# Kernel optimization log

Hardware: AMD Instinct MI355X
Metric: run time of the kernel (lower is better)

Reference implementation:

```python
import jax, jax.numpy as jnp
import numpy as np
from jax import lax

V, E, F, TL, NS, B = 10000, 150, 200, 7, 4, 2048
PAD_IDX = 1
EPS = 1e-5
SLOPE = 0.01  # nn.LeakyReLU default


def leaky(x):
    return jnp.where(x >= 0, x, SLOPE * x)


def conv1d(x, w, b):
    # x [B,Cin,L], w [Cout,Cin,K] -> [B,Cout,L-K+1]
    y = lax.conv_general_dilated(x, w, (1,), 'VALID',
                                 dimension_numbers=('NCH', 'OIH', 'NCH'))
    return y + b[None, :, None]


def batchnorm(x, g, b):
    # training-mode BatchNorm1d over [B,C,L]: stats over (B,L), biased var
    m = jnp.mean(x, axis=(0, 2), keepdims=True)
    v = jnp.mean((x - m) ** 2, axis=(0, 2), keepdims=True)
    return (x - m) * lax.rsqrt(v + EPS) * g[None, :, None] + b[None, :, None]


def setup_inputs() -> dict:
    key = jax.random.key(0)
    ks = jax.random.split(key, 24)
    s = 0.05
    inp = {
        'text': jax.random.randint(ks[0], (NS * TL, B), 0, V, dtype=jnp.int32).astype(jnp.int64) if False else jax.random.randint(ks[0], (NS * TL, B), 0, V),
        'ith_sentence': 4,
        'idx': 1,
        'emb': jax.random.normal(ks[1], (V, E), jnp.float32) * s,
        'gamma': jnp.ones((F,), jnp.float32),
        'beta': jnp.zeros((F,), jnp.float32),
        'conv1_w': jax.random.normal(ks[2], (F, E, 2), jnp.float32) * s,
        'conv1_b': jax.random.normal(ks[3], (F,), jnp.float32) * s,
        'conv2_w': jax.random.normal(ks[4], (F, F, 2), jnp.float32) * s,
        'conv2_b': jax.random.normal(ks[5], (F,), jnp.float32) * s,
        'conv3_w': jax.random.normal(ks[6], (F, F, 3), jnp.float32) * s,
        'conv3_b': jax.random.normal(ks[7], (F,), jnp.float32) * s,
        'conv4_w': jax.random.normal(ks[8], (F, F, 3), jnp.float32) * s,
        'conv4_b': jax.random.normal(ks[9], (F,), jnp.float32) * s,
        'M_w': jax.random.normal(ks[10], (F, 2 * F), jnp.float32) * s,
        'M_b': jax.random.normal(ks[11], (F,), jnp.float32) * s,
        'U_w': jax.random.normal(ks[12], (7, F, F), jnp.float32) * s,
        'U_b': jax.random.normal(ks[13], (7, F), jnp.float32) * s,
        'R_w': jax.random.normal(ks[14], (F, F), jnp.float32) * s,
        'R_b': jax.random.normal(ks[15], (F,), jnp.float32) * s,
        'H_w': jax.random.normal(ks[16], (F, F), jnp.float32) * s,
        'H_b': jax.random.normal(ks[17], (F,), jnp.float32) * s,
        'X_w': jax.random.normal(ks[18], (F, V), jnp.float32) * s,
        'X_b': jax.random.normal(ks[19], (F,), jnp.float32) * s,
        'Y_w': jax.random.normal(ks[20], (V, F), jnp.float32) * s,
        'Y_b': jax.random.normal(ks[21], (V,), jnp.float32) * s,
    }
    return inp


def _forward(text, ith_sentence, emb, gamma, beta,
             conv1_w, conv1_b, conv2_w, conv2_b, conv3_w, conv3_b,
             conv4_w, conv4_b, M_w, M_b, U_w, U_b, R_w, R_b,
             H_w, H_b, X_w, X_b, Y_w, Y_b):
    batch = text.shape[1]
    embedded = jnp.transpose(emb[text], (1, 2, 0))  # [B,E,S]

    # conv encoder per preceding sentence (Python loop over fixed small count)
    vecs = []
    for j in range(1, ith_sentence):
        seg = embedded[:, :, (j - 1) * TL: j * TL]        # [B,E,7]
        o = leaky(batchnorm(conv1d(seg, conv1_w, conv1_b), gamma, beta))  # L=6
        o = leaky(batchnorm(conv1d(o, conv2_w, conv2_b), gamma, beta))    # L=5
        o = leaky(batchnorm(conv1d(o, conv3_w, conv3_b), gamma, beta))    # L=3
        o = leaky(conv1d(o, conv4_w, conv4_b))                            # L=1
        vecs.append(o[:, :, 0])                           # [B,F]

    h = jnp.zeros((batch, F), embedded.dtype)
    for i in range(ith_sentence - 1):
        h = leaky(jnp.concatenate([vecs[i], h], axis=1) @ M_w.T + M_b)

    # u vectors; faithfully reproduce the original's u1-overwrite in the
    # text_len==7 branch: u1 becomes relu(U7(h)); u6,u7 stay un-activated.
    Uh = jnp.einsum('bf,tgf->tbg', h, U_w) + U_b[:, None, :]  # [7,B,F]
    Ur = leaky(Uh)
    u_steps = jnp.stack([Ur[6], Ur[1], Ur[2], Ur[3], Ur[4], Uh[5], Uh[6]])

    h_terms = jnp.einsum('tbf,gf->tbg', u_steps, H_w) + H_b   # [7,B,F]
    targets = lax.dynamic_slice_in_dim(text, (ith_sentence - 1) * TL, TL, 0)  # [7,B]

    XwT = X_w.T  # [V,F]; X(onehot(w)) == XwT[w] + X_b (same math, direct gather)

    def step(carry, xs):
        r, w = carry
        h_term, tgt = xs
        r = leaky(r @ R_w.T + R_b + XwT[w] + X_b + h_term)    # [B,F]
        y = r @ Y_w.T + Y_b                                   # [B,V]
        logp = jax.nn.log_softmax(y, axis=-1)
        loss_t = -jnp.mean(jnp.take_along_axis(logp, tgt[:, None], 1)[:, 0])
        pred = jnp.argmax(y, axis=1)
        correct_t = jnp.sum((pred == tgt).astype(jnp.int32))
        return (r, pred), (loss_t, correct_t)

    w0 = jnp.zeros((batch,), targets.dtype)
    r0 = jnp.zeros((batch, F), h.dtype)
    _, (losses, corrects) = lax.scan(step, (r0, w0), (h_terms, targets))
    return jnp.sum(losses), jnp.sum(corrects)


def reference(text, ith_sentence, idx, emb, gamma, beta,
              conv1_w, conv1_b, conv2_w, conv2_b, conv3_w, conv3_b,
              conv4_w, conv4_b, M_w, M_b, U_w, U_b, R_w, R_b,
              H_w, H_b, X_w, X_b, Y_w, Y_b):
    loss, correct = _forward(text, int(ith_sentence), emb, gamma, beta,
                             conv1_w, conv1_b, conv2_w, conv2_b,
                             conv3_w, conv3_b, conv4_w, conv4_b,
                             M_w, M_b, U_w, U_b, R_w, R_b,
                             H_w, H_b, X_w, X_b, Y_w, Y_b)
    return loss, correct
```

## Files before the change

kernel.cpp:

```cpp
#include <hip/hip_runtime.h>
#include <math.h>

#define V_    10000
#define VP_   10048
#define E_    150
#define F_    200
#define TL_   7
#define B_    2048
#define NSEG_ 3
#define EPS_  1e-5f
#define SLOPE_ 0.01f
#define NB64  (B_/64)
#define NVB   157
#define NYB   1280
#define KQ_   7

typedef unsigned short u16;
typedef __attribute__((ext_vector_type(8))) short bf16x8;
typedef __attribute__((ext_vector_type(4))) float f32x4;

#define SB0() __builtin_amdgcn_sched_barrier(0)

__device__ __forceinline__ float leaky_f(float x){ return x >= 0.f ? x : SLOPE_*x; }
__device__ __forceinline__ u16 bf16_rne(float x){
  unsigned u = __float_as_uint(x);
  unsigned r = (u + 0x7FFFu + ((u>>16)&1u)) >> 16;
  return (u16)r;
}
__device__ __forceinline__ float bf16_to_f(u16 h){ return __uint_as_float(((unsigned)h)<<16); }

__global__ void transpose_k(const float* __restrict__ in, float* __restrict__ out,
                            int R, int C)
{
  __shared__ float tile[32][33];
  const long long bofs = (long long)blockIdx.z * R * C;
  in += bofs; out += bofs;
  const int c0 = blockIdx.x*32, r0 = blockIdx.y*32;
  const int tx = threadIdx.x, ty = threadIdx.y;
  for (int i = ty; i < 32; i += 8) {
    int r = r0 + i, c = c0 + tx;
    if (r < R && c < C) tile[i][tx] = in[(long long)r*C + c];
  }
  __syncthreads();
  for (int i = ty; i < 32; i += 8) {
    int c = c0 + i, r = r0 + tx;
    if (c < C && r < R) out[(long long)c*R + r] = tile[tx][i];
  }
}

__global__ void gather_x0(const int* __restrict__ text, const float* __restrict__ emb,
                          float* __restrict__ X0)
{
  const int b = blockIdx.x*256 + threadIdx.x;
  const int l = blockIdx.y, j = blockIdx.z;
  const int s = j*TL_ + l;
  const int row = text[(long long)s*B_ + b];
  const float* er = emb + (long long)row*E_;
  float* xp = X0 + ((long long)j*E_*TL_ + l)*B_ + b;
  for (int e = 0; e < E_; ++e) xp[(long long)e*TL_*B_] = er[e];
}

struct PWEnt { const float* src; u16* dh; u16* dl; int kstride; int keff; int nq; };
struct PWTab { PWEnt e[14]; };

__global__ void pack_all_w(PWTab tab)
{
  const PWEnt E = tab.e[blockIdx.y];
  const int q = blockIdx.x;
  if (q >= E.nq) return;
  const int f = threadIdx.x;
  union { u16 u[32]; uint4 v[4]; } H, L;
  #pragma unroll
  for (int kk = 0; kk < 32; ++kk) {
    const int k = q*32 + kk;
    const float x = (k < E.keff && f < F_) ? E.src[(size_t)f*E.kstride + k] : 0.f;
    const u16 h = bf16_rne(x);
    H.u[kk] = h;
    L.u[kk] = bf16_rne(x - bf16_to_f(h));
  }
  uint4* dh = (uint4*)(E.dh + ((size_t)q*256 + f)*32);
  uint4* dl = (uint4*)(E.dl + ((size_t)q*256 + f)*32);
  #pragma unroll
  for (int i = 0; i < 4; ++i) { dh[i] = H.v[i]; dl[i] = L.v[i]; }
}

__global__ void pack_x(const float* __restrict__ X, long long xZ,
                       u16* __restrict__ Oh, u16* __restrict__ Ol, long long oZ)
{
  const int q = blockIdx.y, z = blockIdx.z;
  const int b = blockIdx.x*256 + threadIdx.x;
  X  += (size_t)z*xZ;
  Oh += (size_t)z*oZ; Ol += (size_t)z*oZ;
  union { u16 u[32]; uint4 v[4]; } H, L;
  #pragma unroll
  for (int kk = 0; kk < 32; ++kk) {
    const int k = q*32 + kk;
    const float x = (k < F_) ? X[(size_t)k*B_ + b] : 0.f;
    const u16 h = bf16_rne(x);
    H.u[kk] = h;
    L.u[kk] = bf16_rne(x - bf16_to_f(h));
  }
  uint4* dh = (uint4*)(Oh + ((size_t)q*B_ + b)*32);
  uint4* dl = (uint4*)(Ol + ((size_t)q*B_ + b)*32);
  #pragma unroll
  for (int i = 0; i < 4; ++i) { dh[i] = H.v[i]; dl[i] = L.v[i]; }
}

__global__ void us_pack(const float* __restrict__ Uh,
                        u16* __restrict__ Oh, u16* __restrict__ Ol, long long oZ)
{
  const int q = blockIdx.y, t = blockIdx.z;
  const int b = blockIdx.x*256 + threadIdx.x;
  const int src = (t == 0) ? 6 : t;
  const float* U = Uh + (size_t)src*F_*B_;
  Oh += (size_t)t*oZ; Ol += (size_t)t*oZ;
  union { u16 u[32]; uint4 v[4]; } H, L;
  #pragma unroll
  for (int kk = 0; kk < 32; ++kk) {
    const int k = q*32 + kk;
    float x = 0.f;
    if (k < F_) {
      x = U[(size_t)k*B_ + b];
      if (t < 5) x = leaky_f(x);
    }
    const u16 h = bf16_rne(x);
    H.u[kk] = h;
    L.u[kk] = bf16_rne(x - bf16_to_f(h));
  }
  uint4* dh = (uint4*)(Oh + ((size_t)q*B_ + b)*32);
  uint4* dl = (uint4*)(Ol + ((size_t)q*B_ + b)*32);
  #pragma unroll
  for (int i = 0; i < 4; ++i) { dh[i] = H.v[i]; dl[i] = L.v[i]; }
}

struct MFrag { bf16x8 h1[4], l1[4], h2[4], l2[4]; };

template<bool TWO>
__device__ __forceinline__ void m_loadq(MFrag& f, int q,
    const u16* __restrict__ X1h, const u16* __restrict__ X1l,
    const u16* __restrict__ X2h, const u16* __restrict__ X2l,
    int b0, int lr, int g)
{
  #pragma unroll
  for (int nt = 0; nt < 4; ++nt) {
    const size_t o = ((size_t)q*B_ + (b0 + nt*16 + lr))*32 + g*8;
    f.h1[nt] = *(const bf16x8*)(X1h + o);
    f.l1[nt] = *(const bf16x8*)(X1l + o);
    if (TWO) {
      f.h2[nt] = *(const bf16x8*)(X2h + o);
      f.l2[nt] = *(const bf16x8*)(X2l + o);
    }
  }
}

template<bool TWO>
__device__ __forceinline__ void m_mfma_chunk(const MFrag& f, int q,
    const u16* __restrict__ W1h, const u16* __restrict__ W1l,
    const u16* __restrict__ W2h, const u16* __restrict__ W2l,
    int f0, int w, int lr, int g, f32x4 acc[4])
{
  const size_t aoff = ((size_t)q*256 + (f0 + w*16 + lr))*32 + g*8;
  {
    const bf16x8 ah = *(const bf16x8*)(W1h + aoff);
    const bf16x8 al = *(const bf16x8*)(W1l + aoff);
    #pragma unroll
    for (int nt = 0; nt < 4; ++nt) {
      acc[nt] = __builtin_amdgcn_mfma_f32_16x16x32_bf16(ah, f.h1[nt], acc[nt], 0, 0, 0);
      acc[nt] = __builtin_amdgcn_mfma_f32_16x16x32_bf16(ah, f.l1[nt], acc[nt], 0, 0, 0);
      acc[nt] = __builtin_amdgcn_mfma_f32_16x16x32_bf16(al, f.h1[nt], acc[nt], 0, 0, 0);
    }
  }
  if (TWO) {
    const bf16x8 ah = *(const bf16x8*)(W2h + aoff);
    const bf16x8 al = *(const bf16x8*)(W2l + aoff);
    #pragma unroll
    for (int nt = 0; nt < 4; ++nt) {
      acc[nt] = __builtin_amdgcn_mfma_f32_16x16x32_bf16(ah, f.h2[nt], acc[nt], 0, 0, 0);
      acc[nt] = __builtin_amdgcn_mfma_f32_16x16x32_bf16(ah, f.l2[nt], acc[nt], 0, 0, 0);
      acc[nt] = __builtin_amdgcn_mfma_f32_16x16x32_bf16(al, f.h2[nt], acc[nt], 0, 0, 0);
    }
  }
}

template<bool TWO, bool LEAKY, bool OUT_F32, bool OUT_PK>
__global__ __launch_bounds__(256) void mf_gemm(
    const u16* __restrict__ W1h, const u16* __restrict__ W1l, long long wZ,
    const u16* __restrict__ X1h, const u16* __restrict__ X1l, long long xZ,
    const u16* __restrict__ W2h, const u16* __restrict__ W2l,
    const u16* __restrict__ X2h, const u16* __restrict__ X2l,
    const float* __restrict__ bias, long long bZ,
    float* __restrict__ Cf, long long cZ,
    u16* __restrict__ Oh, u16* __restrict__ Ol)
{
  const int z = blockIdx.z;
  W1h += (size_t)z*wZ; W1l += (size_t)z*wZ;
  X1h += (size_t)z*xZ; X1l += (size_t)z*xZ;
  const float* bz = bias + (size_t)z*bZ;
  if (OUT_F32) Cf += (size_t)z*cZ;

  const int f0 = blockIdx.x*64;
  const int b0 = blockIdx.y*64;
  const int tid = threadIdx.x;
  const int w = tid >> 6, l = tid & 63;
  const int lr = l & 15, g = l >> 4;

  __shared__ float T[64][65];

  f32x4 acc[4] = {};
  MFrag fA, fB;
  m_loadq<TWO>(fA, 0, X1h, X1l, X2h, X2l, b0, lr, g);
  #pragma unroll
  for (int q = 0; q < KQ_; ++q) {
    MFrag& cur = (q & 1) ? fB : fA;
    MFrag& nxt = (q & 1) ? fA : fB;
    if (q + 1 < KQ_) m_loadq<TWO>(nxt, q + 1, X1h, X1l, X2h, X2l, b0, lr, g);
    SB0();
    m_mfma_chunk<TWO>(cur, q, W1h, W1l, W2h, W2l, f0, w, lr, g, acc);
    SB0();
  }
  #pragma unroll
  for (int nt = 0; nt < 4; ++nt)
    #pragma unroll
    for (int j = 0; j < 4; ++j)
      T[w*16 + g*4 + j][nt*16 + lr] = acc[nt][j];
  __syncthreads();

  const int ty = tid >> 4, tx = tid & 15;
  #pragma unroll
  for (int i = 0; i < 4; ++i) {
    const int f = f0 + ty*4 + i;
    if (f < F_) {
      const float bb = bz[f];
      #pragma unroll
      for (int j = 0; j < 4; ++j) {
        float v = T[ty*4 + i][tx*4 + j] + bb;
        if (LEAKY) v = leaky_f(v);
        if (OUT_F32) Cf[(size_t)f*B_ + b0 + tx*4 + j] = v;
        T[ty*4 + i][tx*4 + j] = v;
      }
    } else {
      #pragma unroll
      for (int j = 0; j < 4; ++j) T[ty*4 + i][tx*4 + j] = 0.f;
    }
  }
  __syncthreads();

  if (OUT_PK) {
    const int bcol = tid & 63;
    const int kk0 = (tid >> 6)*8;
    #pragma unroll
    for (int qh = 0; qh < 2; ++qh) {
      const int q = (f0 >> 5) + qh;
      if (q >= KQ_) continue;
      union { u16 u[8]; uint4 v2[1]; } H, L;
      #pragma unroll
      for (int u = 0; u < 8; ++u) {
        const float x = T[qh*32 + kk0 + u][bcol];
        const u16 h = bf16_rne(x);
        H.u[u] = h;
        L.u[u] = bf16_rne(x - bf16_to_f(h));
      }
      const size_t off = ((size_t)q*B_ + b0 + bcol)*32 + kk0;
      *(uint4*)(Oh + off) = H.v2[0];
      *(uint4*)(Ol + off) = L.v2[0];
    }
  }
}

template<int KW, int LIN, int NQ, int KEFF, bool BN, bool OUT_LEAKY>
__global__ __launch_bounds__(256) void conv_gemm3(
    const u16* __restrict__ Wh, const u16* __restrict__ Wl,
    const float* __restrict__ Y, long long yZ,
    const float* __restrict__ bnS, const float* __restrict__ bnH,
    const float* __restrict__ bias, float* __restrict__ C, long long cZ, int Lout)
{
  const int z = blockIdx.y;
  Y += (size_t)z*yZ; C += (size_t)z*cZ;
  const float* bs_ = BN ? bnS + (size_t)z*F_ : nullptr;
  const float* bh_ = BN ? bnH + (size_t)z*F_ : nullptr;

  const int c0 = blockIdx.x*64;
  const int tid = threadIdx.x;
  const int w  = tid >> 6;
  const int l  = tid & 63;
  const int lr = l & 15, g = l >> 4;

  const int col_s = tid & 63;
  const int ks    = (tid >> 6)*8;
  const int cg    = c0 + col_s;
  const int ts    = cg >> 11, bcol_s = cg & 2047;

  __shared__ u16 LH[2][64][32];
  __shared__ u16 LL[2][64][32];

  f32x4 acc[4][4] = {};
  float rawA[8], rawB[8];

  {
    const int kb = ks;
    int e = kb / KW, kw = kb - e*KW;
    #pragma unroll
    for (int u = 0; u < 8; ++u) {
      rawA[u] = ((kb + u) < KEFF) ? Y[((size_t)(e*LIN + ts + kw))*B_ + bcol_s] : 0.f;
      ++kw; if (kw == KW) { kw = 0; ++e; }
    }
    union { u16 u[8]; uint4 v; } Hh, Ll;
    e = kb / KW; kw = kb - e*KW;
    #pragma unroll
    for (int u = 0; u < 8; ++u) {
      float x = rawA[u];
      if (BN && (kb + u) < KEFF) x = leaky_f(fmaf(x, bs_[e], bh_[e]));
      const u16 h = bf16_rne(x);
      Hh.u[u] = h; Ll.u[u] = bf16_rne(x - bf16_to_f(h));
      ++kw; if (kw == KW) { kw = 0; ++e; }
    }
    *(uint4*)&LH[0][col_s][ks] = Hh.v;
    *(uint4*)&LL[0][col_s][ks] = Ll.v;
  }
  __syncthreads();

  #pragma unroll
  for (int q = 0; q < NQ; ++q) {
    const int buf = q & 1;
    float (&rw)[8] = (q & 1) ? rawA : rawB;

    if (q + 1 < NQ) {
      const int kb = (q + 1)*32 + ks;
      int e = kb / KW, kw = kb - e*KW;
      #pragma unroll
      for (int u = 0; u < 8; ++u) {
        rw[u] = ((kb + u) < KEFF) ? Y[((size_t)(e*LIN + ts + kw))*B_ + bcol_s] : 0.f;
        ++kw; if (kw == KW) { kw = 0; ++e; }
      }
    }
    SB0();
    {
      bf16x8 bh4[4], bl4[4];
      #pragma unroll
      for (int nt = 0; nt < 4; ++nt) {
        bh4[nt] = *(const bf16x8*)&LH[buf][nt*16 + lr][g*8];
        bl4[nt] = *(const bf16x8*)&LL[buf][nt*16 + lr][g*8];
      }
      bf16x8 ah[4], al[4];
      #pragma unroll
      for (int mt = 0; mt < 4; ++mt) {
        const size_t woff = ((size_t)q*256 + (w*64 + mt*16 + lr))*32 + g*8;
        ah[mt] = *(const bf16x8*)(Wh + woff);
        al[mt] = *(const bf16x8*)(Wl + woff);
      }
      #pragma unroll
      for (int mt = 0; mt < 4; ++mt)
        #pragma unroll
        for (int nt = 0; nt < 4; ++nt) {
          acc[mt][nt] = __builtin_amdgcn_mfma_f32_16x16x32_bf16(ah[mt], bh4[nt], acc[mt][nt], 0, 0, 0);
          acc[mt][nt] = __builtin_amdgcn_mfma_f32_16x16x32_bf16(ah[mt], bl4[nt], acc[mt][nt], 0, 0, 0);
          acc[mt][nt] = __builtin_amdgcn_mfma_f32_16x16x32_bf16(al[mt], bh4[nt], acc[mt][nt], 0, 0, 0);
        }
    }
    SB0();
    if (q + 1 < NQ) {
      const int kb = (q + 1)*32 + ks;
      int e = kb / KW, kw = kb - e*KW;
      union { u16 u[8]; uint4 v; } Hh, Ll;
      #pragma unroll
      for (int u = 0; u < 8; ++u) {
        float x = rw[u];
        if (BN && (kb + u) < KEFF) x = leaky_f(fmaf(x, bs_[e], bh_[e]));
        const u16 h = bf16_rne(x);
        Hh.u[u] = h; Ll.u[u] = bf16_rne(x - bf16_to_f(h));
        ++kw; if (kw == KW) { kw = 0; ++e; }
      }
      *(uint4*)&LH[buf ^ 1][col_s][ks] = Hh.v;
      *(uint4*)&LL[buf ^ 1][col_s][ks] = Ll.v;
    }
    __syncthreads();
  }

  #pragma unroll
  for (int mt = 0; mt < 4; ++mt)
    #pragma unroll
    for (int j = 0; j < 4; ++j) {
      const int f = w*64 + mt*16 + g*4 + j;
      if (f < F_) {
        const float bs = bias[f];
        #pragma unroll
        for (int nt = 0; nt < 4; ++nt) {
          const int col = c0 + nt*16 + lr;
          const int t = col >> 11, b = col & 2047;
          float v = acc[mt][nt][j] + bs;
          if (OUT_LEAKY) v = leaky_f(v);
          C[((size_t)f*Lout + t)*B_ + b] = v;
        }
      }
    }
}

__global__ void bn_stats(const float* __restrict__ Y, int L,
                         const float* __restrict__ gamma, const float* __restrict__ beta,
                         float* __restrict__ scale, float* __restrict__ shift)
{
  const int f = blockIdx.x, j = blockIdx.y;
  const float* p = Y + ((long long)(j*F_ + f))*L*B_;
  const int N = L*B_;
  double s = 0.0, s2 = 0.0;
  for (int i = threadIdx.x; i < N; i += 256) { double x = p[i]; s += x; s2 += x*x; }
  __shared__ double sh1[256], sh2[256];
  sh1[threadIdx.x] = s; sh2[threadIdx.x] = s2;
  __syncthreads();
  for (int off = 128; off; off >>= 1) {
    if (threadIdx.x < off) { sh1[threadIdx.x] += sh1[threadIdx.x+off]; sh2[threadIdx.x] += sh2[threadIdx.x+off]; }
    __syncthreads();
  }
  if (threadIdx.x == 0) {
    const double mean = sh1[0]/N;
    const double var  = sh2[0]/N - mean*mean;
    const float rstd = rsqrtf((float)var + EPS_);
    const float sc = gamma[f]*rstd;
    scale[j*F_+f] = sc;
    shift[j*F_+f] = beta[f] - (float)mean*sc;
  }
}

struct RFrag { bf16x8 h[4], lo[4]; };

__device__ __forceinline__ void r_loadq(RFrag& f, int q,
    const u16* __restrict__ Ah, const u16* __restrict__ Al,
    int b0, int lr, int g)
{
  #pragma unroll
  for (int nt = 0; nt < 4; ++nt) {
    const size_t o = ((size_t)q*B_ + (b0 + nt*16 + lr))*32 + g*8;
    f.h[nt]  = *(const bf16x8*)(Ah + o);
    f.lo[nt] = *(const bf16x8*)(Al + o);
  }
}

__global__ __launch_bounds__(256) void r_step(
    const u16* __restrict__ RWh, const u16* __restrict__ RWl,
    const u16* __restrict__ Ain_h, const u16* __restrict__ Ain_l,
    const float* __restrict__ Rb, const float* __restrict__ XwT,
    const float* __restrict__ Xb, const float* __restrict__ HTt,
    const float4* __restrict__ pm4, const float* __restrict__ rPrev,
    const float* __restrict__ Yw, const float* __restrict__ YbF,
    const int* __restrict__ tgt_prev, float* __restrict__ loss_prev,
    int* __restrict__ corr_prev, int have_prev,
    float* __restrict__ rn, u16* __restrict__ Ahi, u16* __restrict__ Alo)
{
  const int f0 = blockIdx.x*64;
  const int b0 = blockIdx.y*64;
  const int tid = threadIdx.x;
  const int w = tid >> 6, l = tid & 63;
  const int lr = l & 15, g = l >> 4;

  __shared__ float T[64][65];
  __shared__ int w_sm[64];

  if (have_prev) {
    const int rr = l >> 2;
    const int ql = l & 3;
    const int row = b0 + w*16 + rr;
    float M = -INFINITY, S = 0.f; int ai = 0x7fffffff;
    for (int p = ql; p < NVB; p += 4) {
      const float4 qq = pm4[(size_t)p*B_ + row];
      const float mm = qq.x, ss = qq.y;
      const int idx = __float_as_int(qq.z);
      if (mm > M) ai = idx;
      else if (mm == M && idx < ai) ai = idx;
      const float M2 = fmaxf(M, mm);
      const float t1 = (M == -INFINITY) ? 0.f : S*__expf(M - M2);
      S = t1 + ss*__expf(mm - M2);
      M = M2;
    }
    const int tb = tgt_prev[row];
    float td = 0.f;
    for (int f2 = ql; f2 < F_; f2 += 4)
      td = fmaf(rPrev[(size_t)f2*B_ + row], Yw[(size_t)tb*F_ + f2], td);
    #pragma unroll
    for (int off = 1; off <= 2; off <<= 1) {
      td += __shfl_xor(td, off);
      const float om = __shfl_xor(M, off);
      const float os = __shfl_xor(S, off);
      const int   oai = __shfl_xor(ai, off);
      if (om > M) ai = oai;
      else if (om == M && oai < ai) ai = oai;
      const float M2 = fmaxf(M, om);
      const float t1 = (M  == -INFINITY) ? 0.f : S *__expf(M  - M2);
      const float t2 = (om == -INFINITY) ? 0.f : os*__expf(om - M2);
      S = t1 + t2;
      M = M2;
    }
    if (ql == 0) {
      if (blockIdx.x == 0) {
        loss_prev[row] = (M + logf(S)) - (td + YbF[tb]);
        corr_prev[row] = (ai == tb) ? 1 : 0;
      }
      w_sm[w*16 + rr] = ai;
    }
  } else {
    if (l < 16) w_sm[w*16 + l] = 0;
  }

  f32x4 acc[4] = {};
  RFrag fA, fB;
  r_loadq(fA, 0, Ain_h, Ain_l, b0, lr, g);
  #pragma unroll
  for (int q = 0; q < KQ_; ++q) {
    RFrag& cur = (q & 1) ? fB : fA;
    RFrag& nxt = (q & 1) ? fA : fB;
    if (q + 1 < KQ_) r_loadq(nxt, q + 1, Ain_h, Ain_l, b0, lr, g);
    SB0();
    {
      const size_t aoff = ((size_t)q*256 + (f0 + w*16 + lr))*32 + g*8;
      const bf16x8 ah = *(const bf16x8*)(RWh + aoff);
      const bf16x8 al = *(const bf16x8*)(RWl + aoff);
      #pragma unroll
      for (int nt = 0; nt < 4; ++nt) {
        acc[nt] = __builtin_amdgcn_mfma_f32_16x16x32_bf16(ah, cur.h[nt],  acc[nt], 0, 0, 0);
        acc[nt] = __builtin_amdgcn_mfma_f32_16x16x32_bf16(ah, cur.lo[nt], acc[nt], 0, 0, 0);
        acc[nt] = __builtin_amdgcn_mfma_f32_16x16x32_bf16(al, cur.h[nt],  acc[nt], 0, 0, 0);
      }
    }
    SB0();
  }
  #pragma unroll
  for (int nt = 0; nt < 4; ++nt)
    #pragma unroll
    for (int j = 0; j < 4; ++j)
      T[w*16 + g*4 + j][nt*16 + lr] = acc[nt][j];
  __syncthreads();

  const int ty = tid >> 4, tx = tid & 15;
  int wv[4];
  #pragma unroll
  for (int j = 0; j < 4; ++j) {
    int t_ = w_sm[tx*4 + j];
    wv[j] = (t_ < 0) ? 0 : (t_ >= V_ ? V_-1 : t_);
  }

  #pragma unroll
  for (int i = 0; i < 4; ++i) {
    const int f = f0 + ty*4 + i;
    if (f < F_) {
      const float rb = Rb[f] + Xb[f];
      #pragma unroll
      for (int j = 0; j < 4; ++j) {
        const int b = b0 + tx*4 + j;
        float v = T[ty*4 + i][tx*4 + j] + rb + XwT[(size_t)wv[j]*F_ + f] + HTt[(size_t)f*B_ + b];
        v = leaky_f(v);
        rn[(size_t)f*B_ + b] = v;
        T[ty*4 + i][tx*4 + j] = v;
      }
    } else {
      #pragma unroll
      for (int j = 0; j < 4; ++j) T[ty*4 + i][tx*4 + j] = 0.f;
    }
  }
  __syncthreads();

  const int bcol = tid & 63;
  const int kk0 = (tid >> 6)*8;
  #pragma unroll
  for (int qh = 0; qh < 2; ++qh) {
    const int q = (f0 >> 5) + qh;
    if (q >= KQ_) continue;
    union { u16 u[8]; uint4 v2[1]; } H, L;
    #pragma unroll
    for (int u = 0; u < 8; ++u) {
      const float x = T[qh*32 + kk0 + u][bcol];
      const u16 h = bf16_rne(x);
      H.u[u] = h;
      L.u[u] = bf16_rne(x - bf16_to_f(h));
    }
    const size_t off = ((size_t)q*B_ + b0 + bcol)*32 + kk0;
    *(uint4*)(Ahi + off) = H.v2[0];
    *(uint4*)(Alo + off) = L.v2[0];
  }
}

__global__ void pack_yw(const float* __restrict__ Yw, const float* __restrict__ Yb,
                        u16* __restrict__ Bhi, u16* __restrict__ Blo, float* __restrict__ YbP)
{
  const int q = blockIdx.x;
  const int v = blockIdx.y*256 + threadIdx.x;
  if (v >= VP_) return;
  if (q == 0) YbP[v] = (v < V_) ? Yb[v] : -INFINITY;
  union { u16 u[32]; uint4 w[4]; } H, L;
  #pragma unroll
  for (int kk = 0; kk < 32; ++kk) {
    const int f = q*32 + kk;
    const float x = (f < F_ && v < V_) ? Yw[(size_t)v*F_ + f] : 0.f;
    const u16 h = bf16_rne(x);
    H.u[kk] = h;
    L.u[kk] = bf16_rne(x - bf16_to_f(h));
  }
  uint4* dh = (uint4*)(Bhi + ((size_t)q*VP_ + v)*32);
  uint4* dl = (uint4*)(Blo + ((size_t)q*VP_ + v)*32);
  #pragma unroll
  for (int i = 0; i < 4; ++i) { dh[i] = H.w[i]; dl[i] = L.w[i]; }
}

struct YFrag2 { bf16x8 ah[4], al[4], bh[4], bl[4]; };

__device__ __forceinline__ void y_loadq2(YFrag2& f, int q,
    const u16* __restrict__ Ahi, const u16* __restrict__ Alo,
    const u16* __restrict__ Bhi, const u16* __restrict__ Blo,
    int b0, int v0, int w, int lr, int g)
{
  #pragma unroll
  for (int mt = 0; mt < 4; ++mt) {
    const size_t o = ((size_t)q*B_ + (b0 + w*64 + mt*16 + lr))*32 + g*8;
    f.ah[mt] = *(const bf16x8*)(Ahi + o);
    f.al[mt] = *(const bf16x8*)(Alo + o);
  }
  #pragma unroll
  for (int nt = 0; nt < 4; ++nt) {
    const size_t o = ((size_t)q*VP_ + (v0 + nt*16 + lr))*32 + g*8;
    f.bh[nt] = *(const bf16x8*)(Bhi + o);
    f.bl[nt] = *(const bf16x8*)(Blo + o);
  }
}

__device__ __forceinline__ void y_mfmaq2(const YFrag2& f, f32x4 acc[4][4])
{
  #pragma unroll
  for (int mt = 0; mt < 4; ++mt)
    #pragma unroll
    for (int nt = 0; nt < 4; ++nt) {
      acc[mt][nt] = __builtin_amdgcn_mfma_f32_16x16x32_bf16(f.ah[mt], f.bh[nt], acc[mt][nt], 0, 0, 0);
      acc[mt][nt] = __builtin_amdgcn_mfma_f32_16x16x32_bf16(f.ah[mt], f.bl[nt], acc[mt][nt], 0, 0, 0);
      acc[mt][nt] = __builtin_amdgcn_mfma_f32_16x16x32_bf16(f.al[mt], f.bh[nt], acc[mt][nt], 0, 0, 0);
    }
}

__global__ __launch_bounds__(256, 2) void y_mfma(
    const u16* __restrict__ Ahi, const u16* __restrict__ Alo,
    const u16* __restrict__ Bhi, const u16* __restrict__ Blo,
    const float* __restrict__ YbP, float4* __restrict__ pm4)
{
  const int bid = blockIdx.x;
  const int xcd = bid & 7;
  const int i   = bid >> 3;
  const int by  = i & 7;
  const int vb  = xcd*20 + (i >> 3);
  if (vb >= NVB) return;
  const int v0 = vb*64;
  const int b0 = by*256;
  const int w  = threadIdx.x >> 6;
  const int l  = threadIdx.x & 63;
  const int lr = l & 15;
  const int g  = l >> 4;

  f32x4 acc[4][4] = {};

  YFrag2 fA, fB;
  y_loadq2(fA, 0, Ahi, Alo, Bhi, Blo, b0, v0, w, lr, g);
  #pragma unroll
  for (int q = 0; q < KQ_; ++q) {
    YFrag2& cur = (q & 1) ? fB : fA;
    YFrag2& nxt = (q & 1) ? fA : fB;
    if (q + 1 < KQ_)
      y_loadq2(nxt, q + 1, Ahi, Alo, Bhi, Blo, b0, v0, w, lr, g);
    SB0();
    __builtin_amdgcn_s_setprio(1);
    y_mfmaq2(cur, acc);
    __builtin_amdgcn_s_setprio(0);
    SB0();
  }

  float ybv[4];
  #pragma unroll
  for (int nt = 0; nt < 4; ++nt) ybv[nt] = YbP[v0 + nt*16 + lr];

  float m[4][4]; int ai[4][4];
  #pragma unroll
  for (int mt = 0; mt < 4; ++mt)
    #pragma unroll
    for (int j = 0; j < 4; ++j) { m[mt][j] = -INFINITY; ai[mt][j] = 0x7fffffff; }

  #pragma unroll
  for (int nt = 0; nt < 4; ++nt) {
    const int colv = v0 + nt*16 + lr;
    #pragma unroll
    for (int mt = 0; mt < 4; ++mt)
      #pragma unroll
      for (int j = 0; j < 4; ++j) {
        const float y = acc[mt][nt][j] + ybv[nt];
        if (y > m[mt][j]) { m[mt][j] = y; ai[mt][j] = colv; }
      }
  }
  #pragma unroll
  for (int off = 1; off <= 8; off <<= 1) {
    #pragma unroll
    for (int mt = 0; mt < 4; ++mt)
      #pragma unroll
      for (int j = 0; j < 4; ++j) {
        const float om = __shfl_xor(m[mt][j], off);
        const int   oai = __shfl_xor(ai[mt][j], off);
        if (om > m[mt][j] || (om == m[mt][j] && oai < ai[mt][j])) { m[mt][j] = om; ai[mt][j] = oai; }
      }
  }

  float s[4][4] = {};
  #pragma unroll
  for (int nt = 0; nt < 4; ++nt) {
    #pragma unroll
    for (int mt = 0; mt < 4; ++mt)
      #pragma unroll
      for (int j = 0; j < 4; ++j)
        s[mt][j] += __expf(acc[mt][nt][j] + ybv[nt] - m[mt][j]);
  }
  #pragma unroll
  for (int off = 1; off <= 8; off <<= 1) {
    #pragma unroll
    for (int mt = 0; mt < 4; ++mt)
      #pragma unroll
      for (int j = 0; j < 4; ++j)
        s[mt][j] += __shfl_xor(s[mt][j], off);
  }

  if (lr == 0) {
    #pragma unroll
    for (int mt = 0; mt < 4; ++mt)
      #pragma unroll
      for (int j = 0; j < 4; ++j) {
        const int row = b0 + w*64 + mt*16 + g*4 + j;
        pm4[(size_t)vb*B_ + row] = make_float4(m[mt][j], s[mt][j], __int_as_float(ai[mt][j]), 0.f);
      }
  }
}

__global__ void combine2(const float4* __restrict__ pm4,
                         const float* __restrict__ r, const float* __restrict__ Yw,
                         const float* __restrict__ Yb, const int* __restrict__ tgt,
                         int* __restrict__ w, float* __restrict__ loss_row,
                         int* __restrict__ corr_row)
{
  const int b = blockIdx.x*4 + (threadIdx.x >> 6);
  const int lane = threadIdx.x & 63;
  const int tb = tgt[b];

  float td = 0.f;
  #pragma unroll
  for (int it = 0; it < 4; ++it) {
    const int f = lane + it*64;
    if (f < F_) td = fmaf(r[(size_t)f*B_ + b], Yw[(size_t)tb*F_ + f], td);
  }

  float M = -INFINITY, S = 0.f; int ai = 0x7fffffff;
  for (int p = lane; p < NVB; p += 64) {
    const float4 q = pm4[(size_t)p*B_ + b];
    const float mm = q.x, s = q.y;
    const int idx = __float_as_int(q.z);
    if (mm > M) ai = idx;
    else if (mm == M && idx < ai) ai = idx;
    const float M2 = fmaxf(M, mm);
    const float t1 = (M == -INFINITY) ? 0.f : S*__expf(M - M2);
    S = t1 + s*__expf(mm - M2);
    M = M2;
  }
  #pragma unroll
  for (int off = 1; off <= 32; off <<= 1) {
    td += __shfl_xor(td, off);
    const float om = __shfl_xor(M, off);
    const float os = __shfl_xor(S, off);
    const int   oai = __shfl_xor(ai, off);
    if (om > M) ai = oai;
    else if (om == M && oai < ai) ai = oai;
    const float M2 = fmaxf(M, om);
    const float t1 = (M  == -INFINITY) ? 0.f : S *__expf(M  - M2);
    const float t2 = (om == -INFINITY) ? 0.f : os*__expf(om - M2);
    S = t1 + t2;
    M = M2;
  }
  if (lane == 0) {
    const float logZ = M + logf(S);
    loss_row[b] = logZ - (td + Yb[tb]);
    corr_row[b] = (ai == tb) ? 1 : 0;
    w[b] = ai;
  }
}

__global__ void finalize_k(const float* __restrict__ lr, const int* __restrict__ cr,
                           float* __restrict__ out)
{
  __shared__ float sf[256]; __shared__ int si[256];
  float s = 0.f; int c = 0;
  for (int i = threadIdx.x; i < 7*B_; i += 256) { s += lr[i]; c += cr[i]; }
  sf[threadIdx.x] = s; si[threadIdx.x] = c;
  __syncthreads();
  for (int off = 128; off; off >>= 1) {
    if (threadIdx.x < off) { sf[threadIdx.x] += sf[threadIdx.x+off]; si[threadIdx.x] += si[threadIdx.x+off]; }
    __syncthreads();
  }
  if (threadIdx.x == 0) { out[0] = sf[0] / (float)B_; out[1] = (float)si[0]; }
}

extern "C" void kernel_launch(void* const* d_in, const int* in_sizes, int n_in,
                              void* d_out, int out_size, void* d_ws, size_t ws_size,
                              hipStream_t stream)
{
  (void)in_sizes; (void)n_in; (void)out_size; (void)ws_size;
  const int*   text = (const int*)d_in[0];
  const float* emb  = (const float*)d_in[3];
  const float* gamma= (const float*)d_in[4];
  const float* beta = (const float*)d_in[5];
  const float* c1w = (const float*)d_in[6];  const float* c1b = (const float*)d_in[7];
  const float* c2w = (const float*)d_in[8];  const float* c2b = (const float*)d_in[9];
  const float* c3w = (const float*)d_in[10]; const float* c3b = (const float*)d_in[11];
  const float* c4w = (const float*)d_in[12]; const float* c4b = (const float*)d_in[13];
  const float* Mw = (const float*)d_in[14];  const float* Mb = (const float*)d_in[15];
  const float* Uw = (const float*)d_in[16];  const float* Ub = (const float*)d_in[17];
  const float* Rw = (const float*)d_in[18];  const float* Rb = (const float*)d_in[19];
  const float* Hw = (const float*)d_in[20];  const float* Hb = (const float*)d_in[21];
  const float* Xw = (const float*)d_in[22];  const float* Xb = (const float*)d_in[23];
  const float* Yw = (const float*)d_in[24];  const float* Yb = (const float*)d_in[25];

  float* ws = (float*)d_ws;
  size_t off = 0;
  auto alloc = [&](size_t n)->float* { float* p = ws + off; off += (n + 63) & ~(size_t)63; return p; };

  u16* W1h = (u16*)alloc((size_t)10*256*32/2); u16* W1l = (u16*)alloc((size_t)10*256*32/2);
  u16* W2h = (u16*)alloc((size_t)13*256*32/2); u16* W2l = (u16*)alloc((size_t)13*256*32/2);
  u16* W3h = (u16*)alloc((size_t)19*256*32/2); u16* W3l = (u16*)alloc((size_t)19*256*32/2);
  u16* W4h = (u16*)alloc((size_t)19*256*32/2); u16* W4l = (u16*)alloc((size_t)19*256*32/2);
  u16* RWh = (u16*)alloc((size_t)7*256*32/2);  u16* RWl = (u16*)alloc((size_t)7*256*32/2);
  u16* MW1h= (u16*)alloc((size_t)7*256*32/2);  u16* MW1l= (u16*)alloc((size_t)7*256*32/2);
  u16* MW2h= (u16*)alloc((size_t)7*256*32/2);  u16* MW2l= (u16*)alloc((size_t)7*256*32/2);
  u16* UWh = (u16*)alloc((size_t)6*7*256*32/2);u16* UWl = (u16*)alloc((size_t)6*7*256*32/2);
  u16* HWh = (u16*)alloc((size_t)7*256*32/2);  u16* HWl = (u16*)alloc((size_t)7*256*32/2);
  float* S1 = alloc(3*F_); float* Sh1 = alloc(3*F_);
  float* S2 = alloc(3*F_); float* Sh2 = alloc(3*F_);
  float* S3 = alloc(3*F_); float* Sh3 = alloc(3*F_);
  float* YbP = alloc(VP_);
  float* P  = alloc((size_t)NSEG_*E_*TL_*B_);
  float* Q  = alloc((size_t)NSEG_*F_*6*B_);
  float* VEC = alloc((size_t)NSEG_*F_*B_);
  float* rA = alloc((size_t)F_*B_);
  float* rB = alloc((size_t)F_*B_);
  u16* PKh = (u16*)alloc((size_t)13*10240*32/2);
  u16* PKl = (u16*)alloc((size_t)13*10240*32/2);
  int*   wbuf = (int*)alloc(B_);
  float* loss_rows = alloc((size_t)7*B_);
  int*   corr_rows = (int*)alloc((size_t)7*B_);

  float* X0 = P;
  float* Y1 = Q;
  float* Y2 = P;
  float* Y3 = Q;
  float* Uh = Q;
  float* HT = P;

  const size_t HT_FL = (size_t)7*F_*B_;
  u16* YWhi = (u16*)(P + HT_FL);
  u16* YWlo = YWhi + (size_t)KQ_*VP_*32;
  u16* A0h  = YWlo + (size_t)KQ_*VP_*32;
  u16* A0l  = A0h + (size_t)KQ_*B_*32;
  u16* A1h  = A0l + (size_t)KQ_*B_*32;
  u16* A1l  = A1h + (size_t)KQ_*B_*32;

  u16* hAh = (u16*)(Q + (size_t)5734400);
  u16* hAl = hAh + (size_t)KQ_*B_*32;
  u16* hBh = hAl + (size_t)KQ_*B_*32;
  u16* hBl = hBh + (size_t)KQ_*B_*32;

  u16* VPh = PKh;  u16* VPl = PKl;
  u16* USh = PKh;  u16* USl = PKl;

  float4* pm4 = (float4*)Q;
  float*  XwT = Q + (size_t)2097152;

  const long long FRZ = (long long)KQ_*B_*32;
  const long long WQZ = (long long)KQ_*256*32;

  const dim3 tb_(32,8);

  PWTab tab;
  tab.e[0] = { c1w,      W1h,  W1l,  300, 300, 10 };
  tab.e[1] = { c2w,      W2h,  W2l,  400, 400, 13 };
  tab.e[2] = { c3w,      W3h,  W3l,  600, 600, 19 };
  tab.e[3] = { c4w,      W4h,  W4l,  600, 600, 19 };
  tab.e[4] = { Rw,       RWh,  RWl,  200, 200, 7 };
  tab.e[5] = { Mw,       MW1h, MW1l, 400, 200, 7 };
  tab.e[6] = { Mw + 200, MW2h, MW2l, 400, 200, 7 };
  tab.e[7] = { Hw,       HWh,  HWl,  200, 200, 7 };
  for (int i = 0; i < 6; ++i)
    tab.e[8+i] = { Uw + (size_t)(1+i)*F_*F_, UWh + (size_t)i*WQZ, UWl + (size_t)i*WQZ, 200, 200, 7 };
  hipLaunchKernelGGL(pack_all_w, dim3(19, 14), dim3(256), 0, stream, tab);

  hipLaunchKernelGGL(gather_x0, dim3(B_/256, TL_, NSEG_), dim3(256), 0, stream, text, emb, X0);

  hipLaunchKernelGGL((conv_gemm3<2,7,10,300,false,false>), dim3(192,3), dim3(256), 0, stream,
      W1h, W1l, X0, (long long)E_*TL_*B_, nullptr, nullptr, c1b, Y1, (long long)F_*6*B_, 6);
  hipLaunchKernelGGL(bn_stats, dim3(F_, NSEG_), dim3(256), 0, stream, Y1, 6, gamma, beta, S1, Sh1);
  hipLaunchKernelGGL((conv_gemm3<2,6,13,400,true,false>), dim3(160,3), dim3(256), 0, stream,
      W2h, W2l, Y1, (long long)F_*6*B_, S1, Sh1, c2b, Y2, (long long)F_*5*B_, 5);
  hipLaunchKernelGGL(bn_stats, dim3(F_, NSEG_), dim3(256), 0, stream, Y2, 5, gamma, beta, S2, Sh2);
  hipLaunchKernelGGL((conv_gemm3<3,5,19,600,true,false>), dim3(96,3), dim3(256), 0, stream,
      W3h, W3l, Y2, (long long)F_*5*B_, S2, Sh2, c3b, Y3, (long long)F_*3*B_, 3);
  hipLaunchKernelGGL(bn_stats, dim3(F_, NSEG_), dim3(256), 0, stream, Y3, 3, gamma, beta, S3, Sh3);
  hipLaunchKernelGGL((conv_gemm3<3,3,19,600,true,true>), dim3(32,3), dim3(256), 0, stream,
      W4h, W4l, Y3, (long long)F_*3*B_, S3, Sh3, c4b, VEC, (long long)F_*B_, 1);

  hipLaunchKernelGGL(pack_x, dim3(B_/256, KQ_, NSEG_), dim3(256), 0, stream,
      VEC, (long long)F_*B_, VPh, VPl, FRZ);
  hipMemsetAsync(hAh, 0, (size_t)2*KQ_*B_*32*2, stream);
  u16 *hch = hAh, *hcl = hAl, *hnh = hBh, *hnl = hBl;
  for (int i = 0; i < 3; ++i) {
    hipLaunchKernelGGL((mf_gemm<true,true,false,true>), dim3(4, 32, 1), dim3(256), 0, stream,
        MW1h, MW1l, 0, VPh + (size_t)i*FRZ, VPl + (size_t)i*FRZ, 0,
        MW2h, MW2l, hch, hcl, Mb, 0, nullptr, 0, hnh, hnl);
    u16* t1 = hch; hch = hnh; hnh = t1;
    u16* t2 = hcl; hcl = hnl; hnl = t2;
  }

  hipLaunchKernelGGL((mf_gemm<false,false,true,false>), dim3(4, 32, 6), dim3(256), 0, stream,
      UWh, UWl, WQZ, hch, hcl, 0, nullptr, nullptr, nullptr, nullptr,
      Ub + F_, F_, Uh + (size_t)F_*B_, (long long)F_*B_, nullptr, nullptr);
  hipLaunchKernelGGL(us_pack, dim3(B_/256, KQ_, 7), dim3(256), 0, stream,
      Uh, USh, USl, FRZ);
  hipLaunchKernelGGL((mf_gemm<false,false,true,false>), dim3(4, 32, 7), dim3(256), 0, stream,
      HWh, HWl, 0, USh, USl, FRZ, nullptr, nullptr, nullptr, nullptr,
      Hb, 0, HT, (long long)F_*B_, nullptr, nullptr);

  hipLaunchKernelGGL(transpose_k, dim3(313,7,1), tb_, 0, stream, Xw, XwT, F_, V_);
  hipLaunchKernelGGL(pack_yw, dim3(KQ_, (VP_+255)/256), dim3(256), 0, stream, Yw, Yb, YWhi, YWlo, YbP);
  hipMemsetAsync(A0h, 0, (size_t)2*KQ_*B_*32*2, stream);

  u16 *cin_h = A0h, *cin_l = A0l, *cout_h = A1h, *cout_l = A1l;
  float *rOld = rA, *rNew = rB;
  for (int t = 0; t < 7; ++t) {
    const int* tgt_prev = text + (size_t)(20 + t)*B_;
    float* lp = (t > 0) ? loss_rows + (size_t)(t-1)*B_ : loss_rows;
    int*   cp = (t > 0) ? corr_rows + (size_t)(t-1)*B_ : corr_rows;
    hipLaunchKernelGGL(r_step, dim3(4, 32), dim3(256), 0, stream,
        RWh, RWl, cin_h, cin_l, Rb, XwT, Xb, HT + (size_t)t*F_*B_,
        pm4, rOld, Yw, Yb, tgt_prev, lp, cp, (int)(t > 0),
        rNew, cout_h, cout_l);
    hipLaunchKernelGGL(y_mfma, dim3(NYB), dim3(256), 0, stream,
        cout_h, cout_l, YWhi, YWlo, YbP, pm4);
    float* tr = rOld; rOld = rNew; rNew = tr;
    u16* th = cin_h; cin_h = cout_h; cout_h = th;
    u16* tl = cin_l; cin_l = cout_l; cout_l = tl;
  }
  hipLaunchKernelGGL(combine2, dim3(B_/4), dim3(256), 0, stream,
      pm4, rOld, Yw, Yb, text + (size_t)27*B_, wbuf,
      loss_rows + (size_t)6*B_, corr_rows + (size_t)6*B_);

  hipLaunchKernelGGL(finalize_k, dim3(1), dim3(256), 0, stream, loss_rows, corr_rows, (float*)d_out);
}
```

Before: 968.7 us.

## Stage shared Y weight tile in LDS instead of per-wave global loads

In the Y projection MFMA kernel, all four waves previously loaded the same B (Y_w hi/lo) fragments from global memory independently. Now each thread loads a slice of the 64-column B tile into double-buffered LDS, and waves read their fragments from LDS, cutting global B traffic by four. In exchange it adds a __syncthreads per K step, extra LDS reads and writes, and LDS usage that may affect occupancy.

```diff
diff --git a/kernel.cpp b/kernel.cpp
--- a/kernel.cpp
+++ b/kernel.cpp
@@ -599,12 +599,11 @@
   for (int i = 0; i < 4; ++i) { dh[i] = H.w[i]; dl[i] = L.w[i]; }
 }
 
-struct YFrag2 { bf16x8 ah[4], al[4], bh[4], bl[4]; };
-
-__device__ __forceinline__ void y_loadq2(YFrag2& f, int q,
+struct AFr { bf16x8 ah[4], al[4]; };
+
+__device__ __forceinline__ void ya_loadq(AFr& f, int q,
     const u16* __restrict__ Ahi, const u16* __restrict__ Alo,
-    const u16* __restrict__ Bhi, const u16* __restrict__ Blo,
-    int b0, int v0, int w, int lr, int g)
+    int b0, int w, int lr, int g)
 {
   #pragma unroll
   for (int mt = 0; mt < 4; ++mt) {
@@ -612,24 +611,6 @@
     f.ah[mt] = *(const bf16x8*)(Ahi + o);
     f.al[mt] = *(const bf16x8*)(Alo + o);
   }
-  #pragma unroll
-  for (int nt = 0; nt < 4; ++nt) {
-    const size_t o = ((size_t)q*VP_ + (v0 + nt*16 + lr))*32 + g*8;
-    f.bh[nt] = *(const bf16x8*)(Bhi + o);
-    f.bl[nt] = *(const bf16x8*)(Blo + o);
-  }
-}
-
-__device__ __forceinline__ void y_mfmaq2(const YFrag2& f, f32x4 acc[4][4])
-{
-  #pragma unroll
-  for (int mt = 0; mt < 4; ++mt)
-    #pragma unroll
-    for (int nt = 0; nt < 4; ++nt) {
-      acc[mt][nt] = __builtin_amdgcn_mfma_f32_16x16x32_bf16(f.ah[mt], f.bh[nt], acc[mt][nt], 0, 0, 0);
-      acc[mt][nt] = __builtin_amdgcn_mfma_f32_16x16x32_bf16(f.ah[mt], f.bl[nt], acc[mt][nt], 0, 0, 0);
-      acc[mt][nt] = __builtin_amdgcn_mfma_f32_16x16x32_bf16(f.al[mt], f.bh[nt], acc[mt][nt], 0, 0, 0);
-    }
 }
 
 __global__ __launch_bounds__(256, 2) void y_mfma(
@@ -645,26 +626,67 @@
   if (vb >= NVB) return;
   const int v0 = vb*64;
   const int b0 = by*256;
-  const int w  = threadIdx.x >> 6;
-  const int l  = threadIdx.x & 63;
+  const int tid = threadIdx.x;
+  const int w  = tid >> 6;
+  const int l  = tid & 63;
   const int lr = l & 15;
   const int g  = l >> 4;
 
+  const int col_s = tid & 63;
+  const int ks    = (tid >> 6)*8;
+
+  __shared__ u16 LH[2][64][40];
+  __shared__ u16 LL[2][64][40];
+
   f32x4 acc[4][4] = {};
 
-  YFrag2 fA, fB;
-  y_loadq2(fA, 0, Ahi, Alo, Bhi, Blo, b0, v0, w, lr, g);
+  AFr fA, fB;
+  {
+    const size_t bo = ((size_t)(v0 + col_s))*32 + ks;
+    *(uint4*)&LH[0][col_s][ks] = *(const uint4*)(Bhi + bo);
+    *(uint4*)&LL[0][col_s][ks] = *(const uint4*)(Blo + bo);
+  }
+  ya_loadq(fA, 0, Ahi, Alo, b0, w, lr, g);
+  __syncthreads();
+
   #pragma unroll
   for (int q = 0; q < KQ_; ++q) {
-    YFrag2& cur = (q & 1) ? fB : fA;
-    YFrag2& nxt = (q & 1) ? fA : fB;
-    if (q + 1 < KQ_)
-      y_loadq2(nxt, q + 1, Ahi, Alo, Bhi, Blo, b0, v0, w, lr, g);
+    const int buf = q & 1;
+    AFr& cur = (q & 1) ? fB : fA;
+    AFr& nxt = (q & 1) ? fA : fB;
+
+    uint4 sbh, sbl;
+    if (q + 1 < KQ_) {
+      const size_t bo = ((size_t)(q+1)*VP_ + (v0 + col_s))*32 + ks;
+      sbh = *(const uint4*)(Bhi + bo);
+      sbl = *(const uint4*)(Blo + bo);
+      ya_loadq(nxt, q + 1, Ahi, Alo, b0, w, lr, g);
+    }
     SB0();
-    __builtin_amdgcn_s_setprio(1);
-    y_mfmaq2(cur, acc);
-    __builtin_amdgcn_s_setprio(0);
+    {
+      bf16x8 bh4[4], bl4[4];
+      #pragma unroll
+      for (int nt = 0; nt < 4; ++nt) {
+        bh4[nt] = *(const bf16x8*)&LH[buf][nt*16 + lr][g*8];
+        bl4[nt] = *(const bf16x8*)&LL[buf][nt*16 + lr][g*8];
+      }
+      __builtin_amdgcn_s_setprio(1);
+      #pragma unroll
+      for (int mt = 0; mt < 4; ++mt)
+        #pragma unroll
+        for (int nt = 0; nt < 4; ++nt) {
+          acc[mt][nt] = __builtin_amdgcn_mfma_f32_16x16x32_bf16(cur.ah[mt], bh4[nt], acc[mt][nt], 0, 0, 0);
+          acc[mt][nt] = __builtin_amdgcn_mfma_f32_16x16x32_bf16(cur.ah[mt], bl4[nt], acc[mt][nt], 0, 0, 0);
+          acc[mt][nt] = __builtin_amdgcn_mfma_f32_16x16x32_bf16(cur.al[mt], bh4[nt], acc[mt][nt], 0, 0, 0);
+        }
+      __builtin_amdgcn_s_setprio(0);
+    }
     SB0();
+    if (q + 1 < KQ_) {
+      *(uint4*)&LH[buf ^ 1][col_s][ks] = sbh;
+      *(uint4*)&LL[buf ^ 1][col_s][ks] = sbl;
+    }
+    __syncthreads();
   }
 
   float ybv[4];
```

Measured after the change: 933.4 us, median of 2. -3.6%, faster.
